# Kernel optimization log

Measured on AMD Instinct MI355X. Metric: run time of the kernel, lower is better.

The kernel has to match this reference:

```python
import jax, jax.numpy as jnp
import numpy as np

N_NODES = 50000
N_EDGES = 800000
D_IN, D_HID, D_OUT = 128, 64, 64


def gcn_conv(x, W, b, src, dst, num_nodes):
    """PyG-style GCNConv: add self-loops, symmetric norm, aggregate at target.
    src/dst already include self-loops. x: [N, Din], W: [Din, Dout]."""
    xw = x @ W  # transform first (Din -> Dout), like PyG
    ew = jnp.ones(src.shape[0], dtype=x.dtype)
    deg = jax.ops.segment_sum(ew, dst, num_segments=num_nodes)
    dis = jnp.where(deg > 0, jax.lax.rsqrt(deg), 0.0)  # deg^{-1/2}
    norm = dis[src] * ew * dis[dst]  # [E+N]
    msgs = norm[:, None] * xw[src]  # gather source features
    out = jax.ops.segment_sum(msgs, dst, num_segments=num_nodes)
    return out + b


def setup_inputs() -> dict:
    key = jax.random.key(0)
    ks = jax.random.split(key, 8)
    x = jax.random.normal(ks[0], (N_NODES, D_IN), dtype=jnp.float32)
    edge_index = jax.random.randint(ks[1], (2, N_EDGES), 0, N_NODES, dtype=jnp.int64)
    W1 = jax.random.normal(ks[2], (D_IN, D_HID), dtype=jnp.float32) * (1.0 / np.sqrt(D_IN))
    b1 = jnp.zeros((D_HID,), dtype=jnp.float32)
    W2 = jax.random.normal(ks[3], (D_HID, D_HID), dtype=jnp.float32) * (1.0 / np.sqrt(D_HID))
    b2 = jnp.zeros((D_HID,), dtype=jnp.float32)
    W3 = jax.random.normal(ks[4], (D_HID, D_OUT), dtype=jnp.float32) * (1.0 / np.sqrt(D_HID))
    b3 = jnp.zeros((D_OUT,), dtype=jnp.float32)
    return {"x": x, "edge_index": edge_index, "W1": W1, "b1": b1,
            "W2": W2, "b2": b2, "W3": W3, "b3": b3}


def reference(x, edge_index, W1, b1, W2, b2, W3, b3):
    # Add self-loops once (shared by all layers), as PyG GCNConv does per layer.
    loop = jnp.arange(N_NODES, dtype=edge_index.dtype)
    src = jnp.concatenate([edge_index[0], loop])
    dst = jnp.concatenate([edge_index[1], loop])
    # Layer 1 + ReLU (dropout is identity in eval mode)
    h = gcn_conv(x, W1, b1, src, dst, N_NODES)
    h = jax.nn.relu(h)
    # Layer 2 + ReLU
    h = gcn_conv(h, W2, b2, src, dst, N_NODES)
    h = jax.nn.relu(h)
    # Layer 3 (no activation)
    out = gcn_conv(h, W3, b3, src, dst, N_NODES)
    return out
```

## Files before the change

### kernel.cpp

```cpp
#include <hip/hip_runtime.h>
#include <hip/hip_fp16.h>

#define N_NODES 50000
#define N_PAD   50048
#define N_EDGES 800000
#define D_IN    128
#define D_HID   64

#define NB         196
#define EB_CHUNK   4096
#define BIN_BLOCKS 196
#define ESTRIDE    4864
#define CSTRIDE    (ESTRIDE + 256)

typedef __bf16 bf16x8 __attribute__((ext_vector_type(8)));
typedef float  f32x4  __attribute__((ext_vector_type(4)));


template <int K>
__device__ __forceinline__ void pack_w(const float* __restrict__ W,
                                       __bf16* __restrict__ Bh, __bf16* __restrict__ Bl, int i) {
  constexpr int KS = K / 32;
  int j = i & 7, lane = (i >> 3) & 63, rest = i >> 9;
  int ct = rest / KS, ks = rest - ct * KS;
  int k = ks * 32 + ((lane >> 4) << 3) + j;
  int c = ct * 16 + (lane & 15);
  float v = W[k * 64 + c];
  __bf16 hb = (__bf16)v;
  Bh[i] = hb;
  Bl[i] = (__bf16)(v - (float)hb);
}


__global__ __launch_bounds__(256) void k_bins_sw(const int* __restrict__ src,
                                                 const int* __restrict__ dst,
                                                 unsigned* __restrict__ bucket_fill,
                                                 unsigned* __restrict__ temp,
                                                 const float* __restrict__ W1,
                                                 const float* __restrict__ W2,
                                                 const float* __restrict__ W3,
                                                 __bf16* __restrict__ Wh1, __bf16* __restrict__ Wl1,
                                                 __bf16* __restrict__ Wh2, __bf16* __restrict__ Wl2,
                                                 __bf16* __restrict__ Wh3, __bf16* __restrict__ Wl3) {
  __shared__ unsigned lh[256], lcur[256];
  int blk = blockIdx.x, t = threadIdx.x;
  if (blk >= BIN_BLOCKS) {
    int b = blk - BIN_BLOCKS;
    if (b < 32)      pack_w<D_IN >(W1, Wh1, Wl1, b * 256 + t);
    else if (b < 48) pack_w<D_HID>(W2, Wh2, Wl2, (b - 32) * 256 + t);
    else             pack_w<D_HID>(W3, Wh3, Wl3, (b - 48) * 256 + t);
    return;
  }
  lh[t] = 0;
  __syncthreads();
  int base = blk * EB_CHUNK;
  int endv = min(base + EB_CHUNK, N_EDGES);
  for (int e = base + t; e < endv; e += 256)
    atomicAdd(&lh[((unsigned)dst[e]) >> 8], 1u);
  __syncthreads();
  unsigned c = lh[t];
  lcur[t] = t * ESTRIDE + (c ? atomicAdd(&bucket_fill[t], c) : 0u);
  __syncthreads();
  for (int e = base + t; e < endv; e += 256) {
    unsigned d = (unsigned)dst[e];
    unsigned pos = atomicAdd(&lcur[d >> 8], 1u);
    temp[pos] = (unsigned)src[e] | ((d & 255u) << 16);
  }
}


template <int K, bool FIRST>
__device__ __forceinline__ void gemm_body(int bid,
                                          const float* __restrict__ Xf,
                                          const __bf16* __restrict__ Ah,
                                          const __bf16* __restrict__ Al,
                                          const __bf16* __restrict__ Bh,
                                          const __bf16* __restrict__ Bl,
                                          __half* __restrict__ Y) {
  constexpr int KS = K / 32;
  const int tid  = threadIdx.x;
  const int wave = tid >> 6;
  const int lane = tid & 63;
  const int row0 = bid * 64 + wave * 16;
  const int row_a = FIRST ? min(row0 + (lane & 15), N_NODES - 1)
                          : row0 + (lane & 15);
  const int q8 = (lane >> 4) << 3;

  f32x4 acc[4];
#pragma unroll
  for (int ct = 0; ct < 4; ct++) acc[ct] = (f32x4){0.f, 0.f, 0.f, 0.f};

#pragma unroll
  for (int ks = 0; ks < KS; ks++) {
    bf16x8 ah, al;
    if (FIRST) {
      const float4* xr4 = reinterpret_cast<const float4*>(Xf + (size_t)row_a * K);
      float4 f0 = xr4[ks * 8 + (q8 >> 2) + 0];
      float4 f1 = xr4[ks * 8 + (q8 >> 2) + 1];
#pragma unroll
      for (int j = 0; j < 4; j++) {
        float a0 = (&f0.x)[j], a1 = (&f1.x)[j];
        __bf16 h0 = (__bf16)a0, h1 = (__bf16)a1;
        ah[j] = h0;     al[j] = (__bf16)(a0 - (float)h0);
        ah[4 + j] = h1; al[4 + j] = (__bf16)(a1 - (float)h1);
      }
    } else {
      size_t abase = (size_t)row_a * K + q8 + ks * 32;
      ah = *reinterpret_cast<const bf16x8*>(Ah + abase);
      al = *reinterpret_cast<const bf16x8*>(Al + abase);
    }
#pragma unroll
    for (int ct = 0; ct < 4; ct++) {
      bf16x8 bh = *reinterpret_cast<const bf16x8*>(Bh + (size_t)((ct * KS + ks) * 64 + lane) * 8);
      bf16x8 bl = *reinterpret_cast<const bf16x8*>(Bl + (size_t)((ct * KS + ks) * 64 + lane) * 8);
      acc[ct] = __builtin_amdgcn_mfma_f32_16x16x32_bf16(ah, bh, acc[ct], 0, 0, 0);
      acc[ct] = __builtin_amdgcn_mfma_f32_16x16x32_bf16(ah, bl, acc[ct], 0, 0, 0);
      acc[ct] = __builtin_amdgcn_mfma_f32_16x16x32_bf16(al, bh, acc[ct], 0, 0, 0);
    }
  }

  const int rbase = row0 + ((lane >> 4) << 2);
  const int c     = lane & 15;
#pragma unroll
  for (int ct = 0; ct < 4; ct++)
#pragma unroll
    for (int r = 0; r < 4; r++) {
      int row = rbase + r;
      if (row < N_NODES)
        Y[(size_t)row * 64 + ct * 16 + c] = __float2half_rn(acc[ct][r]);
    }
}


__global__ __launch_bounds__(256) void k_csr_gemm1(const unsigned* __restrict__ temp,
                                                   const unsigned* __restrict__ bucket_fill,
                                                   unsigned* __restrict__ rowptr,
                                                   unsigned* __restrict__ rowend,
                                                   float* __restrict__ dis,
                                                   unsigned short* __restrict__ csr,
                                                   const float* __restrict__ x,
                                                   const __bf16* __restrict__ Wh1,
                                                   const __bf16* __restrict__ Wl1,
                                                   __half* __restrict__ xw) {
  __shared__ unsigned hist[256], sscan[256], lfill[256];
  if (blockIdx.x >= NB) {
    gemm_body<D_IN, true>(blockIdx.x - NB, x, nullptr, nullptr, Wh1, Wl1, xw);
    return;
  }
  int b = blockIdx.x, t = threadIdx.x;
  unsigned ebase = b * ESTRIDE, ecnt = bucket_fill[b], cbase = b * CSTRIDE;
  int nodes = min(256, N_NODES - b * 256);
  hist[t] = 0;
  __syncthreads();
  for (unsigned i = t; i < ecnt; i += 256)
    atomicAdd(&hist[(temp[ebase + i] >> 16) & 255u], 1u);
  __syncthreads();
  unsigned deg = (t < nodes) ? hist[t] + 1u : 0u;
  sscan[t] = deg;
  __syncthreads();
  for (int off = 1; off < 256; off <<= 1) {
    unsigned v = (t >= off) ? sscan[t - off] : 0u;
    __syncthreads();
    sscan[t] += v;
    __syncthreads();
  }
  unsigned excl = sscan[t] - deg;
  if (t < nodes) {
    int node = b * 256 + t;
    rowptr[node] = cbase + excl;
    rowend[node] = cbase + excl + deg;
    dis[node] = rsqrtf((float)deg);
    csr[cbase + excl] = (unsigned short)node;
  }
  lfill[t] = excl + 1u;
  __syncthreads();
  for (unsigned i = t; i < ecnt; i += 256) {
    unsigned v = temp[ebase + i];
    unsigned d = (v >> 16) & 255u;
    unsigned pos = atomicAdd(&lfill[d], 1u);
    csr[cbase + pos] = (unsigned short)(v & 0xFFFFu);
  }
}


__global__ __launch_bounds__(256) void k_gemm23(const __bf16* __restrict__ Ah,
                                                const __bf16* __restrict__ Al,
                                                const __bf16* __restrict__ Bh,
                                                const __bf16* __restrict__ Bl,
                                                __half* __restrict__ Y) {
  gemm_body<D_HID, false>(blockIdx.x, nullptr, Ah, Al, Bh, Bl, Y);
}


template <int MODE>
__global__ __launch_bounds__(256) void k_agg(const float4* __restrict__ XW4,
                                             const unsigned* __restrict__ rowptr,
                                             const unsigned* __restrict__ rowend,
                                             const unsigned short* __restrict__ csr,
                                             const float* __restrict__ dis,
                                             const float4* __restrict__ bias4,
                                             __bf16* __restrict__ hh,
                                             __bf16* __restrict__ hl,
                                             float4* __restrict__ OUT4) {
  int node = (int)((blockIdx.x * blockDim.x + threadIdx.x) >> 6);
  int lane = threadIdx.x & 63;
  if (node >= N_NODES) return;
  const int sub = lane & 7;
  const int grp = lane >> 3;

  const float disd = dis[node];
  unsigned beg = rowptr[node], end = rowend[node];
  float acc0[8] = {0,0,0,0,0,0,0,0};
  float acc1[8] = {0,0,0,0,0,0,0,0};

  for (unsigned j = beg; j < end; j += 64) {
    int nj = (int)min(64u, end - j);
    unsigned s = 0u; float nrm = 0.f;
    if (lane < nj) {
      s = csr[j + lane];
      nrm = dis[s] * disd;
    }
    for (int k = 0; k < nj; k += 16) {
      int e0 = k + grp;
      unsigned s0 = (unsigned)__shfl((int)s, e0);
      float    n0 = __shfl(nrm, e0);
      float4 v0 = XW4[(size_t)s0 * 8 + sub];
      const __half2* h0 = reinterpret_cast<const __half2*>(&v0);
#pragma unroll
      for (int q = 0; q < 4; q++) {
        float2 f = __half22float2(h0[q]);
        acc0[2*q]   += n0 * f.x;
        acc0[2*q+1] += n0 * f.y;
      }
      if (k + 8 < nj) {
        int e1 = k + grp + 8;
        unsigned s1 = (unsigned)__shfl((int)s, e1);
        float    n1 = __shfl(nrm, e1);
        float4 v1 = XW4[(size_t)s1 * 8 + sub];
        const __half2* h1 = reinterpret_cast<const __half2*>(&v1);
#pragma unroll
        for (int q = 0; q < 4; q++) {
          float2 f = __half22float2(h1[q]);
          acc1[2*q]   += n1 * f.x;
          acc1[2*q+1] += n1 * f.y;
        }
      }
    }
  }

  float acc[8];
#pragma unroll
  for (int i = 0; i < 8; i++) acc[i] = acc0[i] + acc1[i];
#pragma unroll
  for (int i = 0; i < 8; i++) {
    acc[i] += __shfl_xor(acc[i], 8);
    acc[i] += __shfl_xor(acc[i], 16);
    acc[i] += __shfl_xor(acc[i], 32);
  }

  if (grp == 0) {
    float4 ba = bias4[sub * 2], bb = bias4[sub * 2 + 1];
    acc[0] += ba.x; acc[1] += ba.y; acc[2] += ba.z; acc[3] += ba.w;
    acc[4] += bb.x; acc[5] += bb.y; acc[6] += bb.z; acc[7] += bb.w;
    if (MODE == 0) {
      bf16x8 hv, lv;
#pragma unroll
      for (int i = 0; i < 8; i++) {
        float f = fmaxf(acc[i], 0.f);
        __bf16 hb = (__bf16)f;
        hv[i] = hb;
        lv[i] = (__bf16)(f - (float)hb);
      }
      *reinterpret_cast<bf16x8*>(&hh[(size_t)node * 64 + sub * 8]) = hv;
      *reinterpret_cast<bf16x8*>(&hl[(size_t)node * 64 + sub * 8]) = lv;
    } else {
      float4 o0 = {acc[0], acc[1], acc[2], acc[3]};
      float4 o1 = {acc[4], acc[5], acc[6], acc[7]};
      OUT4[(size_t)node * 16 + sub * 2]     = o0;
      OUT4[(size_t)node * 16 + sub * 2 + 1] = o1;
    }
  }
}


extern "C" void kernel_launch(void* const* d_in, const int* in_sizes, int n_in,
                              void* d_out, int out_size, void* d_ws, size_t ws_size,
                              hipStream_t stream) {
  const float* x    = (const float*)d_in[0];
  const int*   eidx = (const int*)d_in[1];
  const float* W1   = (const float*)d_in[2];
  const float* b1   = (const float*)d_in[3];
  const float* W2   = (const float*)d_in[4];
  const float* b2   = (const float*)d_in[5];
  const float* W3   = (const float*)d_in[6];
  const float* b3   = (const float*)d_in[7];
  float* out = (float*)d_out;

  const int* e_src = eidx;
  const int* e_dst = eidx + N_EDGES;

  size_t off = 0;
  auto alloc = [&](size_t bytes) -> void* {
    void* p = (char*)d_ws + off;
    off += (bytes + 255) & ~(size_t)255;
    return p;
  };
  unsigned*       rowptr = (unsigned*)alloc((size_t)N_NODES * 4);
  unsigned*       rowend = (unsigned*)alloc((size_t)N_NODES * 4);
  float*          dis    = (float*)alloc((size_t)N_NODES * 4);
  unsigned short* csr    = (unsigned short*)alloc((size_t)NB * CSTRIDE * 2);
  unsigned*       temp   = (unsigned*)alloc((size_t)NB * ESTRIDE * 4);
  unsigned*       bfill  = (unsigned*)alloc(256 * 4);
  __half*         xw     = (__half*)alloc((size_t)N_PAD * 64 * 2);
  __bf16*         hhA    = (__bf16*)alloc((size_t)N_PAD * 64 * 2);
  __bf16*         hlA    = (__bf16*)alloc((size_t)N_PAD * 64 * 2);
  __bf16*         hhB    = (__bf16*)alloc((size_t)N_PAD * 64 * 2);
  __bf16*         hlB    = (__bf16*)alloc((size_t)N_PAD * 64 * 2);
  __bf16*         Wh1    = (__bf16*)alloc((size_t)D_IN * 64 * 2);
  __bf16*         Wl1    = (__bf16*)alloc((size_t)D_IN * 64 * 2);
  __bf16*         Wh2    = (__bf16*)alloc((size_t)D_HID * 64 * 2);
  __bf16*         Wl2    = (__bf16*)alloc((size_t)D_HID * 64 * 2);
  __bf16*         Wh3    = (__bf16*)alloc((size_t)D_HID * 64 * 2);
  __bf16*         Wl3    = (__bf16*)alloc((size_t)D_HID * 64 * 2);

  const int gemm_grid = N_PAD / 64;
  const int agg_grid  = (N_NODES * 64 + 255) / 256;

  hipMemsetAsync(bfill, 0, 256 * 4, stream);
  k_bins_sw<<<BIN_BLOCKS + 64, 256, 0, stream>>>(e_src, e_dst, bfill, temp,
                                                 W1, W2, W3, Wh1, Wl1, Wh2, Wl2, Wh3, Wl3);
  k_csr_gemm1<<<NB + gemm_grid, 256, 0, stream>>>(temp, bfill, rowptr, rowend,
                                                  dis, csr, x, Wh1, Wl1, xw);
  k_agg<0><<<agg_grid, 256, 0, stream>>>((const float4*)xw, rowptr, rowend, csr, dis,
                                         (const float4*)b1, hhA, hlA, nullptr);
  k_gemm23<<<gemm_grid, 256, 0, stream>>>(hhA, hlA, Wh2, Wl2, xw);
  k_agg<0><<<agg_grid, 256, 0, stream>>>((const float4*)xw, rowptr, rowend, csr, dis,
                                         (const float4*)b2, hhB, hlB, nullptr);
  k_gemm23<<<gemm_grid, 256, 0, stream>>>(hhB, hlB, Wh3, Wl3, xw);
  k_agg<1><<<agg_grid, 256, 0, stream>>>((const float4*)xw, rowptr, rowend, csr, dis,
                                         (const float4*)b3, nullptr, nullptr, (float4*)out);
}
```

Baseline: 137.4 us.

## Fuse aggregation of layers 1-2 with the following small GEMM

Replaces the separate aggregate kernel and 64x64 GEMM kernel for the hidden layers with one fused kernel. Each 1024-thread block aggregates 16 nodes into shared memory and then runs the split-bf16 MFMA GEMM on those rows. This drops the bf16 hi/lo intermediate writes and re-reads and two kernel launches. In exchange, only 4 of 16 waves do the GEMM phase, and the large blocks with a barrier may lower occupancy. Because xw now ping-pongs between two buffers, the GEMM can read from one while writing the other.

```diff
diff --git a/kernel.cpp b/kernel.cpp
--- a/kernel.cpp
+++ b/kernel.cpp
@@ -72,8 +72,6 @@
 template <int K, bool FIRST>
 __device__ __forceinline__ void gemm_body(int bid,
                                           const float* __restrict__ Xf,
-                                          const __bf16* __restrict__ Ah,
-                                          const __bf16* __restrict__ Al,
                                           const __bf16* __restrict__ Bh,
                                           const __bf16* __restrict__ Bl,
                                           __half* __restrict__ Y) {
@@ -82,8 +80,7 @@
   const int wave = tid >> 6;
   const int lane = tid & 63;
   const int row0 = bid * 64 + wave * 16;
-  const int row_a = FIRST ? min(row0 + (lane & 15), N_NODES - 1)
-                          : row0 + (lane & 15);
+  const int row_a = min(row0 + (lane & 15), N_NODES - 1);
   const int q8 = (lane >> 4) << 3;
 
   f32x4 acc[4];
@@ -93,21 +90,15 @@
 #pragma unroll
   for (int ks = 0; ks < KS; ks++) {
     bf16x8 ah, al;
-    if (FIRST) {
-      const float4* xr4 = reinterpret_cast<const float4*>(Xf + (size_t)row_a * K);
-      float4 f0 = xr4[ks * 8 + (q8 >> 2) + 0];
-      float4 f1 = xr4[ks * 8 + (q8 >> 2) + 1];
-#pragma unroll
-      for (int j = 0; j < 4; j++) {
-        float a0 = (&f0.x)[j], a1 = (&f1.x)[j];
-        __bf16 h0 = (__bf16)a0, h1 = (__bf16)a1;
-        ah[j] = h0;     al[j] = (__bf16)(a0 - (float)h0);
-        ah[4 + j] = h1; al[4 + j] = (__bf16)(a1 - (float)h1);
-      }
-    } else {
-      size_t abase = (size_t)row_a * K + q8 + ks * 32;
-      ah = *reinterpret_cast<const bf16x8*>(Ah + abase);
-      al = *reinterpret_cast<const bf16x8*>(Al + abase);
+    const float4* xr4 = reinterpret_cast<const float4*>(Xf + (size_t)row_a * K);
+    float4 f0 = xr4[ks * 8 + (q8 >> 2) + 0];
+    float4 f1 = xr4[ks * 8 + (q8 >> 2) + 1];
+#pragma unroll
+    for (int j = 0; j < 4; j++) {
+      float a0 = (&f0.x)[j], a1 = (&f1.x)[j];
+      __bf16 h0 = (__bf16)a0, h1 = (__bf16)a1;
+      ah[j] = h0;     al[j] = (__bf16)(a0 - (float)h0);
+      ah[4 + j] = h1; al[4 + j] = (__bf16)(a1 - (float)h1);
     }
 #pragma unroll
     for (int ct = 0; ct < 4; ct++) {
@@ -144,7 +135,7 @@
                                                    __half* __restrict__ xw) {
   __shared__ unsigned hist[256], sscan[256], lfill[256];
   if (blockIdx.x >= NB) {
-    gemm_body<D_IN, true>(blockIdx.x - NB, x, nullptr, nullptr, Wh1, Wl1, xw);
+    gemm_body<D_IN, true>(blockIdx.x - NB, x, Wh1, Wl1, xw);
     return;
   }
   int b = blockIdx.x, t = threadIdx.x;
@@ -183,31 +174,13 @@
 }
 
 
-__global__ __launch_bounds__(256) void k_gemm23(const __bf16* __restrict__ Ah,
-                                                const __bf16* __restrict__ Al,
-                                                const __bf16* __restrict__ Bh,
-                                                const __bf16* __restrict__ Bl,
-                                                __half* __restrict__ Y) {
-  gemm_body<D_HID, false>(blockIdx.x, nullptr, Ah, Al, Bh, Bl, Y);
-}
-
-
-template <int MODE>
-__global__ __launch_bounds__(256) void k_agg(const float4* __restrict__ XW4,
-                                             const unsigned* __restrict__ rowptr,
-                                             const unsigned* __restrict__ rowend,
-                                             const unsigned short* __restrict__ csr,
-                                             const float* __restrict__ dis,
-                                             const float4* __restrict__ bias4,
-                                             __bf16* __restrict__ hh,
-                                             __bf16* __restrict__ hl,
-                                             float4* __restrict__ OUT4) {
-  int node = (int)((blockIdx.x * blockDim.x + threadIdx.x) >> 6);
-  int lane = threadIdx.x & 63;
-  if (node >= N_NODES) return;
-  const int sub = lane & 7;
-  const int grp = lane >> 3;
-
+__device__ __forceinline__ void agg_core(int node, int lane, int sub, int grp,
+                                         const float4* __restrict__ XW4,
+                                         const unsigned* __restrict__ rowptr,
+                                         const unsigned* __restrict__ rowend,
+                                         const unsigned short* __restrict__ csr,
+                                         const float* __restrict__ dis,
+                                         float* __restrict__ accout) {
   const float disd = dis[node];
   unsigned beg = rowptr[node], end = rowend[node];
   float acc0[8] = {0,0,0,0,0,0,0,0};
@@ -248,37 +221,104 @@
     }
   }
 
+#pragma unroll
+  for (int i = 0; i < 8; i++) {
+    float a = acc0[i] + acc1[i];
+    a += __shfl_xor(a, 8);
+    a += __shfl_xor(a, 16);
+    a += __shfl_xor(a, 32);
+    accout[i] = a;
+  }
+}
+
+
+__global__ __launch_bounds__(1024) void k_agg_gemm(const float4* __restrict__ XW4,
+                                                   const unsigned* __restrict__ rowptr,
+                                                   const unsigned* __restrict__ rowend,
+                                                   const unsigned short* __restrict__ csr,
+                                                   const float* __restrict__ dis,
+                                                   const float4* __restrict__ bias4,
+                                                   const __bf16* __restrict__ Bh,
+                                                   const __bf16* __restrict__ Bl,
+                                                   __half* __restrict__ Y) {
+  __shared__ float hld[16][68];
+  const int wave = threadIdx.x >> 6;
+  const int lane = threadIdx.x & 63;
+  const int sub  = lane & 7;
+  const int grp  = lane >> 3;
+  const int node = blockIdx.x * 16 + wave;
+
   float acc[8];
-#pragma unroll
-  for (int i = 0; i < 8; i++) acc[i] = acc0[i] + acc1[i];
-#pragma unroll
-  for (int i = 0; i < 8; i++) {
-    acc[i] += __shfl_xor(acc[i], 8);
-    acc[i] += __shfl_xor(acc[i], 16);
-    acc[i] += __shfl_xor(acc[i], 32);
-  }
+  agg_core(node, lane, sub, grp, XW4, rowptr, rowend, csr, dis, acc);
 
   if (grp == 0) {
     float4 ba = bias4[sub * 2], bb = bias4[sub * 2 + 1];
     acc[0] += ba.x; acc[1] += ba.y; acc[2] += ba.z; acc[3] += ba.w;
     acc[4] += bb.x; acc[5] += bb.y; acc[6] += bb.z; acc[7] += bb.w;
-    if (MODE == 0) {
-      bf16x8 hv, lv;
-#pragma unroll
-      for (int i = 0; i < 8; i++) {
-        float f = fmaxf(acc[i], 0.f);
-        __bf16 hb = (__bf16)f;
-        hv[i] = hb;
-        lv[i] = (__bf16)(f - (float)hb);
+    float4 o0, o1;
+    o0.x = fmaxf(acc[0], 0.f); o0.y = fmaxf(acc[1], 0.f);
+    o0.z = fmaxf(acc[2], 0.f); o0.w = fmaxf(acc[3], 0.f);
+    o1.x = fmaxf(acc[4], 0.f); o1.y = fmaxf(acc[5], 0.f);
+    o1.z = fmaxf(acc[6], 0.f); o1.w = fmaxf(acc[7], 0.f);
+    *reinterpret_cast<float4*>(&hld[wave][sub * 8])     = o0;
+    *reinterpret_cast<float4*>(&hld[wave][sub * 8 + 4]) = o1;
+  }
+  __syncthreads();
+
+  if (wave < 4) {
+    const int ct = wave;
+    const int r16 = lane & 15;
+    const int q8  = (lane >> 4) << 3;
+    f32x4 gacc = (f32x4){0.f, 0.f, 0.f, 0.f};
+#pragma unroll
+    for (int ks = 0; ks < 2; ks++) {
+      float4 f0 = *reinterpret_cast<const float4*>(&hld[r16][ks * 32 + q8]);
+      float4 f1 = *reinterpret_cast<const float4*>(&hld[r16][ks * 32 + q8 + 4]);
+      bf16x8 ah, al;
+#pragma unroll
+      for (int j = 0; j < 4; j++) {
+        float a0 = (&f0.x)[j], a1 = (&f1.x)[j];
+        __bf16 h0 = (__bf16)a0, h1 = (__bf16)a1;
+        ah[j] = h0;     al[j] = (__bf16)(a0 - (float)h0);
+        ah[4 + j] = h1; al[4 + j] = (__bf16)(a1 - (float)h1);
       }
-      *reinterpret_cast<bf16x8*>(&hh[(size_t)node * 64 + sub * 8]) = hv;
-      *reinterpret_cast<bf16x8*>(&hl[(size_t)node * 64 + sub * 8]) = lv;
-    } else {
-      float4 o0 = {acc[0], acc[1], acc[2], acc[3]};
-      float4 o1 = {acc[4], acc[5], acc[6], acc[7]};
-      OUT4[(size_t)node * 16 + sub * 2]     = o0;
-      OUT4[(size_t)node * 16 + sub * 2 + 1] = o1;
-    }
+      bf16x8 bh = *reinterpret_cast<const bf16x8*>(Bh + (size_t)((ct * 2 + ks) * 64 + lane) * 8);
+      bf16x8 bl = *reinterpret_cast<const bf16x8*>(Bl + (size_t)((ct * 2 + ks) * 64 + lane) * 8);
+      gacc = __builtin_amdgcn_mfma_f32_16x16x32_bf16(ah, bh, gacc, 0, 0, 0);
+      gacc = __builtin_amdgcn_mfma_f32_16x16x32_bf16(ah, bl, gacc, 0, 0, 0);
+      gacc = __builtin_amdgcn_mfma_f32_16x16x32_bf16(al, bh, gacc, 0, 0, 0);
+    }
+    const int rbase = blockIdx.x * 16 + ((lane >> 4) << 2);
+    const int c     = lane & 15;
+#pragma unroll
+    for (int r = 0; r < 4; r++)
+      Y[(size_t)(rbase + r) * 64 + ct * 16 + c] = __float2half_rn(gacc[r]);
+  }
+}
+
+
+__global__ __launch_bounds__(256) void k_agg3(const float4* __restrict__ XW4,
+                                              const unsigned* __restrict__ rowptr,
+                                              const unsigned* __restrict__ rowend,
+                                              const unsigned short* __restrict__ csr,
+                                              const float* __restrict__ dis,
+                                              const float4* __restrict__ bias4,
+                                              float4* __restrict__ OUT4) {
+  int node = (int)((blockIdx.x * blockDim.x + threadIdx.x) >> 6);
+  int lane = threadIdx.x & 63;
+  if (node >= N_NODES) return;
+  const int sub = lane & 7;
+  const int grp = lane >> 3;
+
+  float acc[8];
+  agg_core(node, lane, sub, grp, XW4, rowptr, rowend, csr, dis, acc);
+
+  if (grp == 0) {
+    float4 ba = bias4[sub * 2], bb = bias4[sub * 2 + 1];
+    float4 o0 = {acc[0] + ba.x, acc[1] + ba.y, acc[2] + ba.z, acc[3] + ba.w};
+    float4 o1 = {acc[4] + bb.x, acc[5] + bb.y, acc[6] + bb.z, acc[7] + bb.w};
+    OUT4[(size_t)node * 16 + sub * 2]     = o0;
+    OUT4[(size_t)node * 16 + sub * 2 + 1] = o1;
   }
 }
 
@@ -311,11 +351,8 @@
   unsigned short* csr    = (unsigned short*)alloc((size_t)NB * CSTRIDE * 2);
   unsigned*       temp   = (unsigned*)alloc((size_t)NB * ESTRIDE * 4);
   unsigned*       bfill  = (unsigned*)alloc(256 * 4);
-  __half*         xw     = (__half*)alloc((size_t)N_PAD * 64 * 2);
-  __bf16*         hhA    = (__bf16*)alloc((size_t)N_PAD * 64 * 2);
-  __bf16*         hlA    = (__bf16*)alloc((size_t)N_PAD * 64 * 2);
-  __bf16*         hhB    = (__bf16*)alloc((size_t)N_PAD * 64 * 2);
-  __bf16*         hlB    = (__bf16*)alloc((size_t)N_PAD * 64 * 2);
+  __half*         xwA    = (__half*)alloc((size_t)N_PAD * 64 * 2);
+  __half*         xwB    = (__half*)alloc((size_t)N_PAD * 64 * 2);
   __bf16*         Wh1    = (__bf16*)alloc((size_t)D_IN * 64 * 2);
   __bf16*         Wl1    = (__bf16*)alloc((size_t)D_IN * 64 * 2);
   __bf16*         Wh2    = (__bf16*)alloc((size_t)D_HID * 64 * 2);
@@ -323,20 +360,19 @@
   __bf16*         Wh3    = (__bf16*)alloc((size_t)D_HID * 64 * 2);
   __bf16*         Wl3    = (__bf16*)alloc((size_t)D_HID * 64 * 2);
 
-  const int gemm_grid = N_PAD / 64;
-  const int agg_grid  = (N_NODES * 64 + 255) / 256;
+  const int gemm_grid  = N_PAD / 64;
+  const int fused_grid = N_NODES / 16;
+  const int agg_grid   = (N_NODES * 64 + 255) / 256;
 
   hipMemsetAsync(bfill, 0, 256 * 4, stream);
   k_bins_sw<<<BIN_BLOCKS + 64, 256, 0, stream>>>(e_src, e_dst, bfill, temp,
                                                  W1, W2, W3, Wh1, Wl1, Wh2, Wl2, Wh3, Wl3);
   k_csr_gemm1<<<NB + gemm_grid, 256, 0, stream>>>(temp, bfill, rowptr, rowend,
-                                                  dis, csr, x, Wh1, Wl1, xw);
-  k_agg<0><<<agg_grid, 256, 0, stream>>>((const float4*)xw, rowptr, rowend, csr, dis,
-                                         (const float4*)b1, hhA, hlA, nullptr);
-  k_gemm23<<<gemm_grid, 256, 0, stream>>>(hhA, hlA, Wh2, Wl2, xw);
-  k_agg<0><<<agg_grid, 256, 0, stream>>>((const float4*)xw, rowptr, rowend, csr, dis,
-                                         (const float4*)b2, hhB, hlB, nullptr);
-  k_gemm23<<<gemm_grid, 256, 0, stream>>>(hhB, hlB, Wh3, Wl3, xw);
-  k_agg<1><<<agg_grid, 256, 0, stream>>>((const float4*)xw, rowptr, rowend, csr, dis,
-                                         (const float4*)b3, nullptr, nullptr, (float4*)out);
-}
+                                                  dis, csr, x, Wh1, Wl1, xwA);
+  k_agg_gemm<<<fused_grid, 1024, 0, stream>>>((const float4*)xwA, rowptr, rowend, csr, dis,
+                                              (const float4*)b1, Wh2, Wl2, xwB);
+  k_agg_gemm<<<fused_grid, 1024, 0, stream>>>((const float4*)xwB, rowptr, rowend, csr, dis,
+                                              (const float4*)b2, Wh3, Wl3, xwA);
+  k_agg3<<<agg_grid, 256, 0, stream>>>((const float4*)xwA, rowptr, rowend, csr, dis,
+                                       (const float4*)b3, (float4*)out);
+}
```

Result: faster. 125.3 us, median of 2 (-8.8%).
